# Kernel optimization log

Hardware: AMD Instinct MI355X
Metric: run time of the kernel (lower is better)

Reference implementation:

```python
import jax, jax.numpy as jnp
import numpy as np

N, D, E, EDGE_DIM = 8192, 64, 262144, 4


def setup_inputs() -> dict:
    key = jax.random.key(0)
    k1, k2, k3, k4, k5, k6 = jax.random.split(key, 6)
    mag = jax.random.uniform(k1, (N, D), dtype=jnp.float32)
    phase = jax.random.normal(k2, (N, D), dtype=jnp.float32)
    edge_index = jax.random.randint(k3, (2, E), 0, N, dtype=jnp.int64)
    edge_attr = jax.random.normal(k4, (E, EDGE_DIM), dtype=jnp.float32)
    # nn.Linear(edge_dim, hidden_dim): weight [hidden_dim, edge_dim], bias [hidden_dim]
    bound = 1.0 / np.sqrt(EDGE_DIM)
    W = jax.random.uniform(k5, (D, EDGE_DIM), minval=-bound, maxval=bound, dtype=jnp.float32)
    b = jax.random.uniform(k6, (D,), minval=-bound, maxval=bound, dtype=jnp.float32)
    return {"mag": mag, "phase": phase, "edge_index": edge_index,
            "edge_attr": edge_attr, "W": W, "b": b}


def reference(mag, phase, edge_index, edge_attr, W, b):
    # score_ij = sum_d mag_i[d]*mag_j[d]*cos(phase_i[d]-phase_j[d])
    # Via cos(a-b) = cos a cos b + sin a sin b -> two [N,D]@[D,N] matmuls,
    # avoiding the O(N^2 D) intermediate while computing identical math.
    c = mag * jnp.cos(phase)  # [N, D]
    s = mag * jnp.sin(phase)  # [N, D]
    scores = c @ c.T + s @ s.T  # [N, N]
    # edge bias: edge_bias[src, dst] = sum_h Linear(edge_attr)[e, h]
    edge_scores = (edge_attr @ W.T + b).sum(axis=-1)  # [E]
    bias = jnp.zeros((mag.shape[0], mag.shape[0]), dtype=scores.dtype)
    bias = bias.at[edge_index[0], edge_index[1]].set(edge_scores)
    scores = scores + bias
    attn = jax.nn.softmax(scores, axis=1)  # [N, N]
    new_mag = attn @ mag  # [N, D]
    new_phase = attn @ phase  # [N, D]
    return new_mag, new_phase
```

## Files before the change

### kernel.cpp

```cpp
#include <hip/hip_runtime.h>
#include <hip/hip_bf16.h>
#include <cstdint>

#define N_NODES 8192
#define DDIM    64
#define DX      128
#define NEDGE   262144
#define BR      128
#define BC      64
#define SPLITS  8
#define TILES   (N_NODES / BC / SPLITS)
#define RCAP    64
#define MSHIFT  66.0f

typedef float f32x16 __attribute__((ext_vector_type(16)));
typedef short short8 __attribute__((ext_vector_type(8)));

__device__ __forceinline__ short f2bf(float f) {
    union { float f; uint32_t u; } v; v.f = f;
    uint32_t u = v.u;
    uint32_t r = (u + 0x7FFFu + ((u >> 16) & 1u)) >> 16;
    return (short)r;
}
__device__ __forceinline__ float bf2f(short s) {
    union { uint32_t u; float f; } v;
    v.u = ((uint32_t)(uint16_t)s) << 16;
    return v.f;
}

__global__ void cpa_prep_all(const float* __restrict__ mag, const float* __restrict__ phase,
                             const int* __restrict__ ei, const float* __restrict__ ea,
                             const float* __restrict__ W, const float* __restrict__ b,
                             short* __restrict__ Xbf, short* __restrict__ Ybt,
                             float* __restrict__ es, int* __restrict__ cnt,
                             int* __restrict__ keys) {
    __shared__ short tile[64][65];
    __shared__ float wsb[5];
    const int blk = blockIdx.x;
    const int tid = threadIdx.x;
    if (blk < 2048) {
        int idx = blk * 256 + tid;
        int i = idx >> 6, d = idx & 63;
        float m = mag[idx], p = phase[idx];
        Xbf[i * DX + d]      = f2bf(m * __cosf(p));
        Xbf[i * DX + 64 + d] = f2bf(m * __sinf(p));
    } else if (blk < 2304) {
        int bb = blk - 2048;
        int bi = bb >> 1;
        int bc = bb & 1;
        int i0 = bi * 64;
        const float* src = bc ? phase : mag;
        for (int itr = 0; itr < 16; ++itr) {
            int idx = tid + itr * 256;
            int ii = idx >> 6, cc = idx & 63;
            tile[ii][cc] = f2bf(src[(size_t)(i0 + ii) * 64 + cc]);
        }
        __syncthreads();
        for (int itr = 0; itr < 16; ++itr) {
            int idx = tid + itr * 256;
            int cc = idx >> 6, ii = idx & 63;
            Ybt[(size_t)(bc * 64 + cc) * N_NODES + i0 + ii] = tile[ii][cc];
        }
    } else {
        if (tid < 64) {
            float w0 = W[tid * 4 + 0], w1 = W[tid * 4 + 1];
            float w2 = W[tid * 4 + 2], w3 = W[tid * 4 + 3];
            float bb = b[tid];
            #pragma unroll
            for (int o = 32; o > 0; o >>= 1) {
                w0 += __shfl_down(w0, o);
                w1 += __shfl_down(w1, o);
                w2 += __shfl_down(w2, o);
                w3 += __shfl_down(w3, o);
                bb += __shfl_down(bb, o);
            }
            if (tid == 0) { wsb[0] = w0; wsb[1] = w1; wsb[2] = w2; wsb[3] = w3; wsb[4] = bb; }
        }
        __syncthreads();
        int e = (blk - 2304) * 256 + tid;
        float4 a = *(const float4*)(ea + (size_t)e * 4);
        es[e] = a.x * wsb[0] + a.y * wsb[1] + a.z * wsb[2] + a.w * wsb[3] + wsb[4];
        int src = ei[e];
        int dst = ei[NEDGE + e];
        int pos = atomicAdd(&cnt[src], 1);
        if (pos < RCAP) keys[src * RCAP + pos] = (dst << 18) | e;
    }
}

__global__ __launch_bounds__(256) void cpa_sortrows(const int* __restrict__ cnt,
                                                    int* __restrict__ keys) {
    int row  = blockIdx.x * 4 + (threadIdx.x >> 6);
    int lane = threadIdx.x & 63;
    int len  = min(cnt[row], RCAP);
    int base = row * RCAP;
    int v = (lane < len) ? keys[base + lane] : 0x7FFFFFFF;

    #pragma unroll
    for (int k = 2; k <= 64; k <<= 1) {
        #pragma unroll
        for (int j = k >> 1; j >= 1; j >>= 1) {
            int p = __shfl_xor(v, j);
            bool asc = (lane & k) == 0;
            bool low = (lane & j) == 0;
            v = (low == asc) ? min(v, p) : max(v, p);
        }
    }
    int nxt = __shfl_down(v, 1);
    bool dead = (lane + 1 < len) && ((v >> 18) == (nxt >> 18));
    if (lane < len) keys[base + lane] = v | (dead ? 0x80000000 : 0);
}

__global__ __launch_bounds__(512, 4) void cpa_flash(
    const short* __restrict__ Xbf, const short* __restrict__ Ybt,
    const float* __restrict__ es, const int* __restrict__ keys,
    const int* __restrict__ cnt,
    float* __restrict__ lsplit, short* __restrict__ Opart)
{
    __shared__ short Xj[BC][136];
    __shared__ short Yt[DX][72];
    __shared__ short Pl[BR][72];

    const int tid  = threadIdx.x;
    const int lane = tid & 63;
    const int w    = tid >> 6;
    const int l31  = lane & 31;
    const int lh   = lane >> 5;
    const int rg   = w >> 1;
    const int cg   = w & 1;
    const int ocg0 = (w & 1) * 2;

    const int ib = blockIdx.x;
    const int split = blockIdx.y;
    const int i0 = ib * BR;
    const int jstart = split * (N_NODES / SPLITS);

    short8 afrag[8];
    #pragma unroll
    for (int kf = 0; kf < 8; ++kf)
        afrag[kf] = *(const short8*)(Xbf + (size_t)(i0 + rg * 32 + l31) * DX + kf * 16 + lh * 8);

    short8 ones;
    #pragma unroll
    for (int j = 0; j < 8; ++j) ones[j] = (short)0x3F80;

    int cur = 0, rend = 0;
    if (lane < 32) {
        int i = i0 + rg * 32 + l31;
        cur = i * RCAP;
        rend = cur + min(cnt[i], RCAP);
        while (cur < rend) {
            int k = keys[cur];
            if (((k >> 18) & 0x1FFF) >= jstart) break;
            ++cur;
        }
    }

    f32x16 O0, O1, lC;
    #pragma unroll
    for (int r = 0; r < 16; ++r) { O0[r] = 0.f; O1[r] = 0.f; lC[r] = 0.f; }

    for (int tt = 0; tt < TILES; ++tt) {
        const int j0 = jstart + tt * BC;
        for (int itr = 0; itr < 2; ++itr) {
            int idx = tid + itr * 512;
            int r = idx >> 4;
            int c8 = (idx & 15) << 3;
            *(int4*)(&Xj[r][c8]) = *(const int4*)(Xbf + (size_t)(j0 + r) * DX + c8);
        }
        for (int itr = 0; itr < 2; ++itr) {
            int idx = tid + itr * 512;
            int n = idx >> 3;
            int k8 = (idx & 7) << 3;
            *(int4*)(&Yt[n][k8]) = *(const int4*)(Ybt + (size_t)n * N_NODES + j0 + k8);
        }
        __syncthreads();

        f32x16 S;
        #pragma unroll
        for (int r = 0; r < 16; ++r) S[r] = 0.f;
        #pragma unroll
        for (int kf = 0; kf < 8; ++kf) {
            short8 bfrag = *(const short8*)&Xj[cg * 32 + l31][kf * 16 + lh * 8];
            S = __builtin_amdgcn_mfma_f32_32x32x16_bf16(afrag[kf], bfrag, S, 0, 0, 0);
        }
        #pragma unroll
        for (int r = 0; r < 16; ++r) {
            int rowl = 4 * lh + (r & 3) + 8 * (r >> 2);
            Pl[rg * 32 + rowl][cg * 32 + l31] = f2bf(__expf(S[r] - MSHIFT));
        }
        if (lane < 32) {
            const int jend = j0 + BC;
            const int wlo = j0 + cg * 32;
            int c = cur;
            while (c < rend) {
                int k = keys[c];
                int dst = (k >> 18) & 0x1FFF;
                if (dst >= jend) break;
                ++c;
                if (k >= 0) {
                    unsigned cl = (unsigned)(dst - wlo);
                    if (cl < 32u) {
                        short* p = &Pl[rg * 32 + l31][cg * 32 + (int)cl];
                        *p = f2bf(bf2f(*p) * __expf(es[k & 0x3FFFF]));
                    }
                }
            }
            cur = c;
        }
        __syncthreads();

        #pragma unroll
        for (int ks = 0; ks < 4; ++ks) {
            short8 pa  = *(const short8*)&Pl[rg * 32 + l31][ks * 16 + lh * 8];
            short8 yb0 = *(const short8*)&Yt[ocg0 * 32 + l31][ks * 16 + lh * 8];
            short8 yb1 = *(const short8*)&Yt[(ocg0 + 1) * 32 + l31][ks * 16 + lh * 8];
            O0 = __builtin_amdgcn_mfma_f32_32x32x16_bf16(pa, yb0, O0, 0, 0, 0);
            O1 = __builtin_amdgcn_mfma_f32_32x32x16_bf16(pa, yb1, O1, 0, 0, 0);
            if (!(w & 1))
                lC = __builtin_amdgcn_mfma_f32_32x32x16_bf16(pa, ones, lC, 0, 0, 0);
        }
        __syncthreads();
    }

    #pragma unroll
    for (int r = 0; r < 16; ++r) {
        int row = rg * 32 + 4 * lh + (r & 3) + 8 * (r >> 2);
        size_t base = ((size_t)split * N_NODES + i0 + row) * DX;
        Opart[base + ocg0 * 32 + l31]       = f2bf(O0[r]);
        Opart[base + (ocg0 + 1) * 32 + l31] = f2bf(O1[r]);
    }
    if (!(w & 1) && l31 == 0) {
        #pragma unroll
        for (int r = 0; r < 16; ++r) {
            int row = rg * 32 + 4 * lh + (r & 3) + 8 * (r >> 2);
            lsplit[(size_t)split * N_NODES + i0 + row] = lC[r];
        }
    }
}

__global__ void cpa_merge(const float* __restrict__ lsplit, const short* __restrict__ Opart,
                          float* __restrict__ out) {
    int gid = blockIdx.x * 256 + threadIdx.x;
    int i = gid >> 7;
    int c = gid & 127;
    float den = 0.f, num = 0.f;
    #pragma unroll
    for (int s = 0; s < SPLITS; ++s) {
        den += lsplit[(size_t)s * N_NODES + i];
        num += bf2f(Opart[((size_t)s * N_NODES + i) * DX + c]);
    }
    float val = num / den;
    if (c < 64) out[(size_t)i * 64 + c] = val;
    else        out[(size_t)N_NODES * 64 + (size_t)i * 64 + (c - 64)] = val;
}

extern "C" void kernel_launch(void* const* d_in, const int* in_sizes, int n_in,
                              void* d_out, int out_size, void* d_ws, size_t ws_size,
                              hipStream_t stream)
{
    const float* mag   = (const float*)d_in[0];
    const float* phase = (const float*)d_in[1];
    const int*   ei    = (const int*)d_in[2];
    const float* ea    = (const float*)d_in[3];
    const float* W     = (const float*)d_in[4];
    const float* b     = (const float*)d_in[5];
    float* out = (float*)d_out;

    char* ws = (char*)d_ws;
    short* Xbf    = (short*)(ws + 0);
    short* Ybt    = (short*)(ws + 2097152);
    float* es     = (float*)(ws + 4194304);
    int*   keys   = (int*)  (ws + 5242880);
    int*   cnt    = (int*)  (ws + 7340032);
    float* lsplit = (float*)(ws + 7373056);
    short* Opart  = (short*)(ws + 7635200);

    hipMemsetAsync(cnt, 0, N_NODES * sizeof(int), stream);
    cpa_prep_all<<<2048 + 256 + NEDGE / 256, 256, 0, stream>>>(mag, phase, ei, ea, W, b,
                                                               Xbf, Ybt, es, cnt, keys);
    cpa_sortrows<<<N_NODES / 4, 256, 0, stream>>>(cnt, keys);
    cpa_flash<<<dim3(N_NODES / BR, SPLITS), 512, 0, stream>>>(Xbf, Ybt, es, keys, cnt,
                                                              lsplit, Opart);
    cpa_merge<<<N_NODES * DX / 256, 256, 0, stream>>>(lsplit, Opart, out);
}
```

Before: 167.8 us.

## Pack edge bias into sorted keys and preload per-row keys into registers

```diff
diff --git a/kernel.cpp b/kernel.cpp
--- a/kernel.cpp
+++ b/kernel.cpp
@@ -88,6 +88,7 @@
 }
 
 __global__ __launch_bounds__(256) void cpa_sortrows(const int* __restrict__ cnt,
+                                                    const float* __restrict__ es,
                                                     int* __restrict__ keys) {
     int row  = blockIdx.x * 4 + (threadIdx.x >> 6);
     int lane = threadIdx.x & 63;
@@ -107,13 +108,23 @@
     }
     int nxt = __shfl_down(v, 1);
     bool dead = (lane + 1 < len) && ((v >> 18) == (nxt >> 18));
-    if (lane < len) keys[base + lane] = v | (dead ? 0x80000000 : 0);
-}
-
-__global__ __launch_bounds__(512, 4) void cpa_flash(
+    int packed;
+    if (lane < len) {
+        int dst = (v >> 18) & 0x1FFF;
+        int e   = v & 0x3FFFF;
+        unsigned esb = (unsigned)(unsigned short)f2bf(es[e]);
+        packed = (dst << 16) | (int)esb | (dead ? (int)0x80000000 : 0);
+    } else {
+        packed = (int)0x80000000;
+    }
+    keys[base + lane] = packed;
+}
+
+__global__ __launch_bounds__(512)
+__attribute__((amdgpu_waves_per_eu(4, 4)))
+void cpa_flash(
     const short* __restrict__ Xbf, const short* __restrict__ Ybt,
-    const float* __restrict__ es, const int* __restrict__ keys,
-    const int* __restrict__ cnt,
+    const int* __restrict__ keys,
     float* __restrict__ lsplit, short* __restrict__ Opart)
 {
     __shared__ short Xj[BC][136];
@@ -143,17 +154,10 @@
     #pragma unroll
     for (int j = 0; j < 8; ++j) ones[j] = (short)0x3F80;
 
-    int cur = 0, rend = 0;
-    if (lane < 32) {
-        int i = i0 + rg * 32 + l31;
-        cur = i * RCAP;
-        rend = cur + min(cnt[i], RCAP);
-        while (cur < rend) {
-            int k = keys[cur];
-            if (((k >> 18) & 0x1FFF) >= jstart) break;
-            ++cur;
-        }
-    }
+    int kreg[32];
+    #pragma unroll
+    for (int r = 0; r < 32; ++r)
+        kreg[r] = keys[(size_t)(i0 + rg * 32 + r) * RCAP + lane];
 
     f32x16 O0, O1, lC;
     #pragma unroll
@@ -188,24 +192,19 @@
             int rowl = 4 * lh + (r & 3) + 8 * (r >> 2);
             Pl[rg * 32 + rowl][cg * 32 + l31] = f2bf(__expf(S[r] - MSHIFT));
         }
-        if (lane < 32) {
-            const int jend = j0 + BC;
+        {
             const int wlo = j0 + cg * 32;
-            int c = cur;
-            while (c < rend) {
-                int k = keys[c];
-                int dst = (k >> 18) & 0x1FFF;
-                if (dst >= jend) break;
-                ++c;
+            #pragma unroll
+            for (int r = 0; r < 32; ++r) {
+                int k = kreg[r];
                 if (k >= 0) {
-                    unsigned cl = (unsigned)(dst - wlo);
+                    unsigned cl = (unsigned)(((k >> 16) & 0x1FFF) - wlo);
                     if (cl < 32u) {
-                        short* p = &Pl[rg * 32 + l31][cg * 32 + (int)cl];
-                        *p = f2bf(bf2f(*p) * __expf(es[k & 0x3FFFF]));
+                        short* p = &Pl[rg * 32 + r][cg * 32 + (int)cl];
+                        *p = f2bf(bf2f(*p) * __expf(bf2f((short)(k & 0xFFFF))));
                     }
                 }
             }
-            cur = c;
         }
         __syncthreads();
 
@@ -278,8 +277,8 @@
     hipMemsetAsync(cnt, 0, N_NODES * sizeof(int), stream);
     cpa_prep_all<<<2048 + 256 + NEDGE / 256, 256, 0, stream>>>(mag, phase, ei, ea, W, b,
                                                                Xbf, Ybt, es, cnt, keys);
-    cpa_sortrows<<<N_NODES / 4, 256, 0, stream>>>(cnt, keys);
-    cpa_flash<<<dim3(N_NODES / BR, SPLITS), 512, 0, stream>>>(Xbf, Ybt, es, keys, cnt,
+    cpa_sortrows<<<N_NODES / 4, 256, 0, stream>>>(cnt, es, keys);
+    cpa_flash<<<dim3(N_NODES / BR, SPLITS), 512, 0, stream>>>(Xbf, Ybt, keys,
                                                               lsplit, Opart);
     cpa_merge<<<N_NODES * DX / 256, 256, 0, stream>>>(lsplit, Opart, out);
 }
```

Result: slower. 249.1 us (+48.4%).

## Replace global row sort with per-block LDS edge lists in flash kernel

Applied to the files above, without the earlier changes.

```diff
diff --git a/kernel.cpp b/kernel.cpp
--- a/kernel.cpp
+++ b/kernel.cpp
@@ -1,5 +1,6 @@
 #include <hip/hip_runtime.h>
 #include <hip/hip_bf16.h>
+#include <hip/hip_fp16.h>
 #include <cstdint>
 
 #define N_NODES 8192
@@ -10,7 +11,9 @@
 #define BC      64
 #define SPLITS  8
 #define TILES   (N_NODES / BC / SPLITS)
+#define SPLW    (N_NODES / SPLITS)
 #define RCAP    64
+#define LCAP    32
 #define MSHIFT  66.0f
 
 typedef float f32x16 __attribute__((ext_vector_type(16)));
@@ -87,29 +90,6 @@
     }
 }
 
-__global__ __launch_bounds__(256) void cpa_sortrows(const int* __restrict__ cnt,
-                                                    int* __restrict__ keys) {
-    int row  = blockIdx.x * 4 + (threadIdx.x >> 6);
-    int lane = threadIdx.x & 63;
-    int len  = min(cnt[row], RCAP);
-    int base = row * RCAP;
-    int v = (lane < len) ? keys[base + lane] : 0x7FFFFFFF;
-
-    #pragma unroll
-    for (int k = 2; k <= 64; k <<= 1) {
-        #pragma unroll
-        for (int j = k >> 1; j >= 1; j >>= 1) {
-            int p = __shfl_xor(v, j);
-            bool asc = (lane & k) == 0;
-            bool low = (lane & j) == 0;
-            v = (low == asc) ? min(v, p) : max(v, p);
-        }
-    }
-    int nxt = __shfl_down(v, 1);
-    bool dead = (lane + 1 < len) && ((v >> 18) == (nxt >> 18));
-    if (lane < len) keys[base + lane] = v | (dead ? 0x80000000 : 0);
-}
-
 __global__ __launch_bounds__(512, 4) void cpa_flash(
     const short* __restrict__ Xbf, const short* __restrict__ Ybt,
     const float* __restrict__ es, const int* __restrict__ keys,
@@ -119,6 +99,8 @@
     __shared__ short Xj[BC][136];
     __shared__ short Yt[DX][72];
     __shared__ short Pl[BR][72];
+    __shared__ int   lkeys[BR][LCAP];
+    __shared__ int   lcnt[BR];
 
     const int tid  = threadIdx.x;
     const int lane = tid & 63;
@@ -132,7 +114,7 @@
     const int ib = blockIdx.x;
     const int split = blockIdx.y;
     const int i0 = ib * BR;
-    const int jstart = split * (N_NODES / SPLITS);
+    const int jstart = split * SPLW;
 
     short8 afrag[8];
     #pragma unroll
@@ -143,17 +125,49 @@
     #pragma unroll
     for (int j = 0; j < 8; ++j) ones[j] = (short)0x3F80;
 
-    int cur = 0, rend = 0;
-    if (lane < 32) {
-        int i = i0 + rg * 32 + l31;
-        cur = i * RCAP;
-        rend = cur + min(cnt[i], RCAP);
-        while (cur < rend) {
-            int k = keys[cur];
-            if (((k >> 18) & 0x1FFF) >= jstart) break;
-            ++cur;
-        }
-    }
+    if (tid < BR) lcnt[tid] = 0;
+    __syncthreads();
+    #pragma unroll
+    for (int k = 0; k < 16; ++k) {
+        int idx = tid + k * 512;
+        int r = idx >> 6, s = idx & 63;
+        int i = i0 + r;
+        if (s < min(cnt[i], RCAP)) {
+            int v = keys[(size_t)i * RCAP + s];
+            int dst = (v >> 18) & 0x1FFF;
+            unsigned drel = (unsigned)(dst - jstart);
+            if (drel < (unsigned)SPLW) {
+                int pos = atomicAdd(&lcnt[r], 1);
+                if (pos < LCAP) lkeys[r][pos] = ((int)drel << 18) | (v & 0x3FFFF);
+            }
+        }
+    }
+    __syncthreads();
+    if (cg == 0 && lane < 32) {
+        int r = rg * 32 + l31;
+        int n = min(lcnt[r], LCAP);
+        lcnt[r] = n;
+        unsigned deadmask = 0;
+        for (int i2 = 0; i2 < n; ++i2) {
+            int vi = lkeys[r][i2];
+            int di = vi >> 18, ei = vi & 0x3FFFF;
+            for (int j2 = 0; j2 < n; ++j2) {
+                int vj = lkeys[r][j2];
+                if ((vj >> 18) == di && (vj & 0x3FFFF) > ei) { deadmask |= 1u << i2; break; }
+            }
+        }
+        for (int i2 = 0; i2 < n; ++i2) {
+            int vi = lkeys[r][i2];
+            if (deadmask & (1u << i2)) {
+                lkeys[r][i2] = (int)0x80000000;
+            } else {
+                union { __half h; unsigned short u; } cv;
+                cv.h = __float2half(es[vi & 0x3FFFF]);
+                lkeys[r][i2] = ((vi >> 18) << 16) | (int)cv.u;
+            }
+        }
+    }
+    __syncthreads();
 
     f32x16 O0, O1, lC;
     #pragma unroll
@@ -189,23 +203,21 @@
             Pl[rg * 32 + rowl][cg * 32 + l31] = f2bf(__expf(S[r] - MSHIFT));
         }
         if (lane < 32) {
-            const int jend = j0 + BC;
-            const int wlo = j0 + cg * 32;
-            int c = cur;
-            while (c < rend) {
-                int k = keys[c];
-                int dst = (k >> 18) & 0x1FFF;
-                if (dst >= jend) break;
-                ++c;
+            int r = rg * 32 + l31;
+            const int tlo = tt * BC + cg * 32;
+            int n = lcnt[r];
+            for (int j2 = 0; j2 < n; ++j2) {
+                int k = lkeys[r][j2];
                 if (k >= 0) {
-                    unsigned cl = (unsigned)(dst - wlo);
+                    unsigned cl = (unsigned)((k >> 16) - tlo);
                     if (cl < 32u) {
-                        short* p = &Pl[rg * 32 + l31][cg * 32 + (int)cl];
-                        *p = f2bf(bf2f(*p) * __expf(es[k & 0x3FFFF]));
+                        union { __half h; unsigned short u; } cv;
+                        cv.u = (unsigned short)(k & 0xFFFF);
+                        short* p = &Pl[r][cg * 32 + (int)cl];
+                        *p = f2bf(bf2f(*p) * __expf(__half2float(cv.h)));
                     }
                 }
             }
-            cur = c;
         }
         __syncthreads();
 
@@ -278,7 +290,6 @@
     hipMemsetAsync(cnt, 0, N_NODES * sizeof(int), stream);
     cpa_prep_all<<<2048 + 256 + NEDGE / 256, 256, 0, stream>>>(mag, phase, ei, ea, W, b,
                                                                Xbf, Ybt, es, cnt, keys);
-    cpa_sortrows<<<N_NODES / 4, 256, 0, stream>>>(cnt, keys);
     cpa_flash<<<dim3(N_NODES / BR, SPLITS), 512, 0, stream>>>(Xbf, Ybt, es, keys, cnt,
                                                               lsplit, Opart);
     cpa_merge<<<N_NODES * DX / 256, 256, 0, stream>>>(lsplit, Opart, out);
```

Result: slower. 179.7 us (+7.1%).
